# Performance work log

Hardware: AMD Instinct MI355X
Metric: run time of the kernel (lower is better)

## Reference

```python
import jax, jax.numpy as jnp
import numpy as np
from jax import lax

T, IN, H, OUT = 8192, 1, 1024, 1


def setup_inputs() -> dict:
    key = jax.random.key(0)
    ks = jax.random.split(key, 7)
    s = 1.0 / np.sqrt(H)
    return {
        "x": jax.random.normal(ks[0], (T, IN), dtype=jnp.float32),
        "W_ih": jax.random.uniform(ks[1], (4 * H, IN), jnp.float32, -s, s),
        "W_hh": jax.random.uniform(ks[2], (4 * H, H), jnp.float32, -s, s),
        "b_ih": jax.random.uniform(ks[3], (4 * H,), jnp.float32, -s, s),
        "b_hh": jax.random.uniform(ks[4], (4 * H,), jnp.float32, -s, s),
        "W_fc": jax.random.uniform(ks[5], (OUT, H), jnp.float32, -s, s),
        "b_fc": jax.random.uniform(ks[6], (OUT,), jnp.float32, -s, s),
    }


def reference(x, W_ih, W_hh, b_ih, b_hh, W_fc, b_fc):
    # x: (T, input_size); batch dim of 1 is squeezed out.
    H_ = W_hh.shape[1]
    # Precompute input contribution to all gates for every timestep: (T, 4H)
    xg = x @ W_ih.T + (b_ih + b_hh)

    def step(carry, gx):
        h, c = carry
        g = gx + h @ W_hh.T  # (4H,) -- PyTorch gate order i, f, g, o
        i, f, gg, o = jnp.split(g, 4)
        c = jax.nn.sigmoid(f) * c + jax.nn.sigmoid(i) * jnp.tanh(gg)
        h = jax.nn.sigmoid(o) * jnp.tanh(c)
        return (h, c), h

    h0 = jnp.zeros((H_,), dtype=x.dtype)
    c0 = jnp.zeros((H_,), dtype=x.dtype)
    _, hs = lax.scan(step, (h0, c0), xg)  # hs: (T, H)
    return hs @ W_fc.T + b_fc  # (T, output_size)
```

## Files before the change

kernel.cpp:

```cpp
#include <hip/hip_runtime.h>

#define TT   8192
#define HD   1024
#define NBLK 256
#define NTHR 256
#define NREP 8

typedef float f32x4 __attribute__((ext_vector_type(4)));
typedef int   i32x4 __attribute__((ext_vector_type(4)));
typedef int   i32x2 __attribute__((ext_vector_type(2)));

__device__ __forceinline__ void llc_load_pair(const unsigned* p, i32x4& a, i32x4& b) {
  asm volatile("global_load_dwordx4 %0, %2, off sc0 sc1\n\t"
               "global_load_dwordx4 %1, %3, off sc0 sc1\n\t"
               "s_waitcnt vmcnt(0)"
               : "=&v"(a), "=&v"(b)
               : "v"(p), "v"(p + 4)
               : "memory");
}
__device__ __forceinline__ unsigned llc_load1(const unsigned* p) {
  unsigned r;
  asm volatile("global_load_dword %0, %1, off sc0 sc1\n\ts_waitcnt vmcnt(0)"
               : "=v"(r) : "v"(p) : "memory");
  return r;
}
__device__ __forceinline__ void llc_store2(unsigned* p, unsigned lo, unsigned hi) {
  i32x2 v; v.x = (int)lo; v.y = (int)hi;
  asm volatile("global_store_dwordx2 %0, %1, off sc0 sc1"
               :: "v"(p), "v"(v) : "memory");
}
__device__ __forceinline__ void llc_store1(unsigned* p, unsigned v) {
  asm volatile("global_store_dword %0, %1, off sc0 sc1"
               :: "v"(p), "v"(v) : "memory");
}

__device__ __forceinline__ float sigf(float z) {
  return 1.0f / (1.0f + __expf(-z));
}
__device__ __forceinline__ float tanh_fast(float z) {
  float az = fabsf(z);
  float e  = __expf(2.0f * az);
  float t  = 1.0f - 2.0f / (e + 1.0f);
  return z < 0.0f ? -t : t;
}

#define FMA4(acc, hvv, wvv)                                      \
  acc = fmaf((hvv).x, (wvv).x, acc);                             \
  acc = fmaf((hvv).y, (wvv).y, acc);                             \
  acc = fmaf((hvv).z, (wvv).z, acc);                             \
  acc = fmaf((hvv).w, (wvv).w, acc);

extern "C" __global__ __launch_bounds__(NTHR, 1)
void lstm_persistent(const float* __restrict__ x,
                     const float* __restrict__ W_ih,
                     const float* __restrict__ W_hh,
                     const float* __restrict__ b_ih,
                     const float* __restrict__ b_hh,
                     const float* __restrict__ W_fc,
                     const float* __restrict__ b_fc,
                     float* __restrict__ out,
                     unsigned* __restrict__ flag,
                     unsigned* __restrict__ hbuf)
{
  __shared__ float x_lds[TT];
  __shared__ float h_lds[HD];

  const int tid  = threadIdx.x;
  const int wave = tid >> 6;
  const int lane = tid & 63;
  const int g    = lane >> 4;
  const int kc   = lane & 15;
  const int blk  = blockIdx.x;
  const int unit = blk * 4 + wave;

  for (int i = tid; i < TT / 4; i += NTHR)
    ((float4*)x_lds)[i] = ((const float4*)x)[i];

  float4 w4[16];
  {
    const float* wr = W_hh + (size_t)(g * HD + unit) * HD + kc * 4;
#pragma unroll
    for (int m = 0; m < 16; ++m)
      w4[m] = *((const float4*)(wr + m * 64));
  }
  float4 wfc4[4];
#pragma unroll
  for (int m = 0; m < 4; ++m)
    wfc4[m] = *((const float4*)(W_fc + m * 256 + lane * 4));
  const float bfc_val = b_fc[0];

  float wih_g[4], bs_g[4];
#pragma unroll
  for (int q = 0; q < 4; ++q) {
    int r = q * HD + unit;
    wih_g[q] = W_ih[r];
    bs_g[q]  = b_ih[r] + b_hh[r];
  }
  float c_state = 0.0f;
  __syncthreads();

  const unsigned* flag_mine = flag + ((blk & (NREP - 1)) << 4);

  for (int t = 0; t < TT; ++t) {
    const bool doproj = (t > 0) && (wave == 1) && (blk == (t & 255));
    float accs = 0.0f;
    float4 hp4[4];

    if (t > 0) {
      if (blk != 0) {
        while (llc_load1(flag_mine) < (unsigned)t) { }
        const unsigned* src = hbuf + ((size_t)((t - 1) & 1) * HD + tid * 4) * 2;
        i32x4 A, B;
        do {
          llc_load_pair(src, A, B);
        } while (!(A.y == t && A.w == t && B.y == t && B.w == t));
        float4 hv;
        hv.x = __int_as_float(A.x); hv.y = __int_as_float(A.z);
        hv.z = __int_as_float(B.x); hv.w = __int_as_float(B.z);
        ((float4*)h_lds)[tid] = hv;
        __syncthreads();
      }

      const float* hp = h_lds + kc * 4;
      float s0 = 0.f, s1 = 0.f, s2 = 0.f, s3 = 0.f;
#pragma unroll
      for (int mb = 0; mb < 4; ++mb) {
        float4 ha = *((const float4*)(hp + (mb * 4 + 0) * 64));
        float4 hb = *((const float4*)(hp + (mb * 4 + 1) * 64));
        float4 hc = *((const float4*)(hp + (mb * 4 + 2) * 64));
        float4 hd = *((const float4*)(hp + (mb * 4 + 3) * 64));
        FMA4(s0, ha, w4[mb * 4 + 0]);
        FMA4(s1, hb, w4[mb * 4 + 1]);
        FMA4(s2, hc, w4[mb * 4 + 2]);
        FMA4(s3, hd, w4[mb * 4 + 3]);
      }
      accs = (s0 + s1) + (s2 + s3);

      if (doproj) {
#pragma unroll
        for (int m = 0; m < 4; ++m)
          hp4[m] = *((const float4*)(h_lds + m * 256 + lane * 4));
      }
    }

#pragma unroll
    for (int s = 1; s < 16; s <<= 1)
      accs += __shfl_xor(accs, s);

    float gi = __shfl(accs, 0);
    float gf = __shfl(accs, 16);
    float gg = __shfl(accs, 32);
    float go = __shfl(accs, 48);

    if (lane == 0) {
      float xt = x_lds[t];
      gi += fmaf(xt, wih_g[0], bs_g[0]);
      gf += fmaf(xt, wih_g[1], bs_g[1]);
      gg += fmaf(xt, wih_g[2], bs_g[2]);
      go += fmaf(xt, wih_g[3], bs_g[3]);
      c_state  = sigf(gf) * c_state + sigf(gi) * tanh_fast(gg);
      float hn = sigf(go) * tanh_fast(c_state);
      llc_store2(hbuf + ((size_t)(t & 1) * HD + unit) * 2,
                 __float_as_uint(hn), (unsigned)(t + 1));
    }

    if (blk == 0) {
      __syncthreads();
      const unsigned* src = hbuf + ((size_t)(t & 1) * HD + tid * 4) * 2;
      i32x4 A, B;
      do {
        llc_load_pair(src, A, B);
      } while (!(A.y == t + 1 && A.w == t + 1 && B.y == t + 1 && B.w == t + 1));
      float4 hv;
      hv.x = __int_as_float(A.x); hv.y = __int_as_float(A.z);
      hv.z = __int_as_float(B.x); hv.w = __int_as_float(B.z);
      ((float4*)h_lds)[tid] = hv;
      __syncthreads();
      if (tid < NREP)
        llc_store1(flag + (tid << 4), (unsigned)(t + 1));
    }

    if (doproj) {
      float p = 0.f;
#pragma unroll
      for (int m = 0; m < 4; ++m) { FMA4(p, hp4[m], wfc4[m]); }
#pragma unroll
      for (int s = 1; s < 64; s <<= 1) p += __shfl_xor(p, s);
      if (lane == 0) out[t - 1] = p + bfc_val;
    }
  }

  if (blk == 0 && wave == 1) {
    float p = 0.f;
#pragma unroll
    for (int m = 0; m < 4; ++m) {
      float4 hm = *((const float4*)(h_lds + m * 256 + lane * 4));
      FMA4(p, hm, wfc4[m]);
    }
#pragma unroll
    for (int s = 1; s < 64; s <<= 1) p += __shfl_xor(p, s);
    if (lane == 0) out[TT - 1] = p + bfc_val;
  }
}

extern "C" void kernel_launch(void* const* d_in, const int* in_sizes, int n_in,
                              void* d_out, int out_size, void* d_ws, size_t ws_size,
                              hipStream_t stream) {
  const float* x   = (const float*)d_in[0];
  const float* Wih = (const float*)d_in[1];
  const float* Whh = (const float*)d_in[2];
  const float* bih = (const float*)d_in[3];
  const float* bhh = (const float*)d_in[4];
  const float* Wfc = (const float*)d_in[5];
  const float* bfc = (const float*)d_in[6];
  float* out = (float*)d_out;

  unsigned* flag = (unsigned*)d_ws;
  unsigned* hbuf = flag + NREP * 16;
  size_t init_bytes = (NREP * 16 + 2 * HD * 2) * sizeof(unsigned);

  hipMemsetAsync(d_ws, 0, init_bytes, stream);
  hipLaunchKernelGGL(lstm_persistent, dim3(NBLK), dim3(NTHR), 0, stream,
                     x, Wih, Whh, bih, bhh, Wfc, bfc, out, flag, hbuf);
}
```

Measured before the change: 23.89 ms.

## Use dedicated coordinator block and 64 wide compute blocks for LSTM recurrence

The layout changes from 256 blocks of 256 threads to 64 compute blocks of 1024 threads, so each block owns 16 hidden units. A separate block 0 now only polls the step tags and publishes the per-step flag. The h exchange buffer grows to four slots and each thread polls a single value/tag pair instead of two 16-byte pairs. The aim is fewer blocks contending on the grid-wide barrier and no compute work on the coordinator's critical path, at the cost of more waves per block and a launch_bounds(NTHR,1) that may now limit registers for the 16 float4 weight tiles per thread.

```diff
diff --git a/kernel.cpp b/kernel.cpp
--- a/kernel.cpp
+++ b/kernel.cpp
@@ -1,28 +1,26 @@
 #include <hip/hip_runtime.h>
 
-#define TT   8192
-#define HD   1024
-#define NBLK 256
-#define NTHR 256
-#define NREP 8
-
-typedef float f32x4 __attribute__((ext_vector_type(4)));
-typedef int   i32x4 __attribute__((ext_vector_type(4)));
-typedef int   i32x2 __attribute__((ext_vector_type(2)));
-
-__device__ __forceinline__ void llc_load_pair(const unsigned* p, i32x4& a, i32x4& b) {
-  asm volatile("global_load_dwordx4 %0, %2, off sc0 sc1\n\t"
-               "global_load_dwordx4 %1, %3, off sc0 sc1\n\t"
-               "s_waitcnt vmcnt(0)"
-               : "=&v"(a), "=&v"(b)
-               : "v"(p), "v"(p + 4)
-               : "memory");
-}
+#define TT    8192
+#define HD    1024
+#define NCB   64
+#define NTHR  1024
+#define NBUF  4
+#define NREP  8
+
+typedef int i32x2 __attribute__((ext_vector_type(2)));
+
 __device__ __forceinline__ unsigned llc_load1(const unsigned* p) {
   unsigned r;
   asm volatile("global_load_dword %0, %1, off sc0 sc1\n\ts_waitcnt vmcnt(0)"
                : "=v"(r) : "v"(p) : "memory");
   return r;
+}
+__device__ __forceinline__ void llc_load_pair8(const unsigned* p,
+                                               unsigned& v, unsigned& tg) {
+  i32x2 r;
+  asm volatile("global_load_dwordx2 %0, %1, off sc0 sc1\n\ts_waitcnt vmcnt(0)"
+               : "=v"(r) : "v"(p) : "memory");
+  v = (unsigned)r.x; tg = (unsigned)r.y;
 }
 __device__ __forceinline__ void llc_store2(unsigned* p, unsigned lo, unsigned hi) {
   i32x2 v; v.x = (int)lo; v.y = (int)hi;
@@ -66,12 +64,25 @@
   __shared__ float h_lds[HD];
 
   const int tid  = threadIdx.x;
+  const int blk  = blockIdx.x;
+
+  if (blk == 0) {
+    for (int t = 0; t < TT; ++t) {
+      const unsigned* tagp = hbuf + (((t & (NBUF - 1)) * HD + tid) * 2 + 1);
+      while (llc_load1(tagp) < (unsigned)(t + 1)) { }
+      __syncthreads();
+      if (tid < NREP)
+        llc_store1(flag + (tid << 4), (unsigned)(t + 1));
+    }
+    return;
+  }
+
+  const int cb   = blk - 1;
   const int wave = tid >> 6;
   const int lane = tid & 63;
   const int g    = lane >> 4;
   const int kc   = lane & 15;
-  const int blk  = blockIdx.x;
-  const int unit = blk * 4 + wave;
+  const int unit = cb * 16 + wave;
 
   for (int i = tid; i < TT / 4; i += NTHR)
     ((float4*)x_lds)[i] = ((const float4*)x)[i];
@@ -99,27 +110,22 @@
   float c_state = 0.0f;
   __syncthreads();
 
-  const unsigned* flag_mine = flag + ((blk & (NREP - 1)) << 4);
+  const unsigned* flag_mine = flag + ((cb & (NREP - 1)) << 4);
 
   for (int t = 0; t < TT; ++t) {
-    const bool doproj = (t > 0) && (wave == 1) && (blk == (t & 255));
+    const bool doproj = (t > 0) && (wave == 1) && (cb == (t & 63));
     float accs = 0.0f;
     float4 hp4[4];
 
     if (t > 0) {
-      if (blk != 0) {
-        while (llc_load1(flag_mine) < (unsigned)t) { }
-        const unsigned* src = hbuf + ((size_t)((t - 1) & 1) * HD + tid * 4) * 2;
-        i32x4 A, B;
-        do {
-          llc_load_pair(src, A, B);
-        } while (!(A.y == t && A.w == t && B.y == t && B.w == t));
-        float4 hv;
-        hv.x = __int_as_float(A.x); hv.y = __int_as_float(A.z);
-        hv.z = __int_as_float(B.x); hv.w = __int_as_float(B.z);
-        ((float4*)h_lds)[tid] = hv;
-        __syncthreads();
-      }
+      while (llc_load1(flag_mine) < (unsigned)t) { }
+      const unsigned* src = hbuf + (((t - 1) & (NBUF - 1)) * HD + tid) * 2;
+      unsigned v, tg;
+      do {
+        llc_load_pair8(src, v, tg);
+      } while (tg != (unsigned)t);
+      h_lds[tid] = __uint_as_float(v);
+      __syncthreads();
 
       const float* hp = h_lds + kc * 4;
       float s0 = 0.f, s1 = 0.f, s2 = 0.f, s3 = 0.f;
@@ -160,24 +166,8 @@
       go += fmaf(xt, wih_g[3], bs_g[3]);
       c_state  = sigf(gf) * c_state + sigf(gi) * tanh_fast(gg);
       float hn = sigf(go) * tanh_fast(c_state);
-      llc_store2(hbuf + ((size_t)(t & 1) * HD + unit) * 2,
+      llc_store2(hbuf + (((t & (NBUF - 1)) * HD + unit) * 2),
                  __float_as_uint(hn), (unsigned)(t + 1));
-    }
-
-    if (blk == 0) {
-      __syncthreads();
-      const unsigned* src = hbuf + ((size_t)(t & 1) * HD + tid * 4) * 2;
-      i32x4 A, B;
-      do {
-        llc_load_pair(src, A, B);
-      } while (!(A.y == t + 1 && A.w == t + 1 && B.y == t + 1 && B.w == t + 1));
-      float4 hv;
-      hv.x = __int_as_float(A.x); hv.y = __int_as_float(A.z);
-      hv.z = __int_as_float(B.x); hv.w = __int_as_float(B.z);
-      ((float4*)h_lds)[tid] = hv;
-      __syncthreads();
-      if (tid < NREP)
-        llc_store1(flag + (tid << 4), (unsigned)(t + 1));
     }
 
     if (doproj) {
@@ -190,16 +180,25 @@
     }
   }
 
-  if (blk == 0 && wave == 1) {
-    float p = 0.f;
-#pragma unroll
-    for (int m = 0; m < 4; ++m) {
-      float4 hm = *((const float4*)(h_lds + m * 256 + lane * 4));
-      FMA4(p, hm, wfc4[m]);
-    }
-#pragma unroll
-    for (int s = 1; s < 64; s <<= 1) p += __shfl_xor(p, s);
-    if (lane == 0) out[TT - 1] = p + bfc_val;
+  if (cb == 0) {
+    const unsigned* src = hbuf + (((TT - 1) & (NBUF - 1)) * HD + tid) * 2;
+    unsigned v, tg;
+    do {
+      llc_load_pair8(src, v, tg);
+    } while (tg != (unsigned)TT);
+    h_lds[tid] = __uint_as_float(v);
+    __syncthreads();
+    if (wave == 1) {
+      float p = 0.f;
+#pragma unroll
+      for (int m = 0; m < 4; ++m) {
+        float4 hm = *((const float4*)(h_lds + m * 256 + lane * 4));
+        FMA4(p, hm, wfc4[m]);
+      }
+#pragma unroll
+      for (int s = 1; s < 64; s <<= 1) p += __shfl_xor(p, s);
+      if (lane == 0) out[TT - 1] = p + bfc_val;
+    }
   }
 }
 
@@ -217,9 +216,9 @@
 
   unsigned* flag = (unsigned*)d_ws;
   unsigned* hbuf = flag + NREP * 16;
-  size_t init_bytes = (NREP * 16 + 2 * HD * 2) * sizeof(unsigned);
+  size_t init_bytes = (NREP * 16 + NBUF * HD * 2) * sizeof(unsigned);
 
   hipMemsetAsync(d_ws, 0, init_bytes, stream);
-  hipLaunchKernelGGL(lstm_persistent, dim3(NBLK), dim3(NTHR), 0, stream,
+  hipLaunchKernelGGL(lstm_persistent, dim3(NCB + 1), dim3(NTHR), 0, stream,
                      x, Wih, Whh, bih, bhh, Wfc, bfc, out, flag, hbuf);
 }
```

Result: slower. 71.77 ms (+200.4%).
